# Kernel tuning notes

Hardware: AMD Instinct MI355X
Metric: run time of the kernel (lower is better)

Reference implementation:

```python
import jax, jax.numpy as jnp
import numpy as np

# SSD prior config (small VGGLite-style)
FEATURE_MAPS = [10, 5, 3, 1]
BOXES_PER_LOC = [4, 4, 4, 4]
IMG = 128      # ssd_config.DATA.SHAPE[0] -> WhereTransformer image_size
OBJ = 64
ZWHAT = 64
HID = 512
B = 4
N_OBJ = sum(f * f for f in FEATURE_MAPS)                       # 135
N_FEAT = sum(b * f * f for f, b in zip(FEATURE_MAPS, BOXES_PER_LOC))  # 540


def reconstruction_indices():
    # Replicates Decoder.reconstruction_indices: map per-location latents to per-box slots.
    idx = []
    last = 0
    for f, bpl in zip(FEATURE_MAPS, BOXES_PER_LOC):
        for i in range(f * f):
            idx.extend([last + i] * bpl)
        last += f * f
    return np.asarray(idx, dtype=np.int32)


def what_decode(z, W1, b1, W2, b2):
    # WhatDecoder: MLP z_what -> 3xOBJxOBJ object glyph in (0,1)
    h = jax.nn.relu(z @ W1 + b1)
    return jax.nn.sigmoid(h @ W2 + b2).reshape(-1, 3, OBJ, OBJ)


def where_stn(imgs, zw):
    # WhereTransformer: paste each object image into its (cx, cy, w, h) box on an IMGxIMG canvas
    # via inverse-affine bilinear sampling with zero padding (STN / grid_sample semantics).
    cx, cy, w, h = zw[:, 0], zw[:, 1], zw[:, 2], zw[:, 3]
    w = jnp.maximum(w, 1e-2)
    h = jnp.maximum(h, 1e-2)
    lin = jnp.linspace(-1.0, 1.0, IMG)
    gy, gx = jnp.meshgrid(lin, lin, indexing='ij')           # (IMG, IMG)
    u = (gx[None] - (2.0 * cx - 1.0)[:, None, None]) / w[:, None, None]
    v = (gy[None] - (2.0 * cy - 1.0)[:, None, None]) / h[:, None, None]
    px = (u + 1.0) * 0.5 * (OBJ - 1)                          # (N, IMG, IMG)
    py = (v + 1.0) * 0.5 * (OBJ - 1)

    def sample_one(img, py, px):  # img: (3, OBJ, OBJ)
        x0 = jnp.floor(px); y0 = jnp.floor(py)
        wx = px - x0; wy = py - y0
        x0i = x0.astype(jnp.int32); y0i = y0.astype(jnp.int32)

        def tap(yi, xi, wgt):
            valid = (yi >= 0) & (yi < OBJ) & (xi >= 0) & (xi < OBJ)
            yc = jnp.clip(yi, 0, OBJ - 1)
            xc = jnp.clip(xi, 0, OBJ - 1)
            return img[:, yc, xc] * (wgt * valid)[None]

        return (tap(y0i, x0i, (1 - wy) * (1 - wx)) + tap(y0i, x0i + 1, (1 - wy) * wx)
                + tap(y0i + 1, x0i, wy * (1 - wx)) + tap(y0i + 1, x0i + 1, wy * wx))

    return jax.vmap(sample_one)(imgs, py, px)                 # (N, 3, IMG, IMG)


def setup_inputs() -> dict:
    key = jax.random.key(0)
    ks = jax.random.split(key, 8)
    return {
        'z_what': jax.random.normal(ks[0], (B, N_OBJ, ZWHAT), jnp.float32),
        'z_where': jax.random.uniform(ks[1], (B, N_FEAT, 4), jnp.float32),
        'z_depth': jax.random.normal(ks[2], (B, N_OBJ, 1), jnp.float32),
        'W1': jax.random.normal(ks[3], (ZWHAT, HID), jnp.float32) * 0.05,
        'b1': jnp.zeros((HID,), jnp.float32),
        'W2': jax.random.normal(ks[4], (HID, 3 * OBJ * OBJ), jnp.float32) * 0.02,
        'b2': jnp.zeros((3 * OBJ * OBJ,), jnp.float32),
        'z_present': jax.random.randint(ks[5], (B, N_FEAT, 1), 0, 2, jnp.int32),
    }


def reference(z_what, z_where, z_depth, W1, b1, W2, b2, z_present):
    idx = jnp.asarray(reconstruction_indices())
    # index_select: replicate per-location latents across boxes-per-location
    zw_full = z_what[:, idx]                                  # (B, N_FEAT, ZWHAT)
    zd_full = z_depth[:, idx]                                 # (B, N_FEAT, 1)
    # sort descending by depth; gather all latents in that order
    order = jnp.argsort(-zd_full[..., 0], axis=1)             # (B, N_FEAT)
    s_what = jnp.take_along_axis(zw_full, order[..., None], axis=1)
    s_where = jnp.take_along_axis(z_where, order[..., None], axis=1)
    s_pres = jnp.take_along_axis(z_present, order[..., None], axis=1)
    # decode + STN warp all objects; absent objects are zeroed (equivalent to the
    dec = what_decode(s_what.reshape(-1, ZWHAT), W1, b1, W2, b2)
    warped = where_stn(dec, s_where.reshape(-1, 4))
    imgs = warped.reshape(B, N_FEAT, 3, IMG, IMG) * s_pres.astype(warped.dtype)[..., None, None]
    # depth compositing: per channel-pixel, take the first nonzero value in sorted order
    nz = imgs != 0
    first = jnp.argmax(nz, axis=1)                            # (B, 3, IMG, IMG)
    out = jnp.take_along_axis(imgs, first[:, None], axis=1)[:, 0] * nz.any(axis=1)
    return out
```

## Files before the change

kernel.cpp:

```cpp
#include <hip/hip_runtime.h>
#include <hip/hip_bf16.h>
#include <math.h>

#define NBOX  540
#define NOBJ  135
#define ZW    64
#define HIDN  512
#define NOUT  12288
#define OBJS  64
#define BATCH 4

#define ROLE_WIN   256
#define ROLE_G1    540
#define ROLE_CVT   ((NOUT / 64) * (HIDN / 64))
#define PRE_BLOCKS (ROLE_WIN + ROLE_G1 + ROLE_CVT)

#define OFF_NROWS  0u
#define OFF_USED   256u
#define OFF_REMAP  2560u
#define OFF_ROWOBJ 4864u
#define OFF_PXWIN  7680u
#define OFF_HBF    269824u
#define OFF_W2T    925184u
#define OFF_DEC    13508096u

typedef short  bf16x8 __attribute__((ext_vector_type(8)));
typedef float  f32x4  __attribute__((ext_vector_type(4)));

struct F4 { float x, y, z, w; };

#define GLOAD_LDS16(gp, lp)                                                    \
  __builtin_amdgcn_global_load_lds(                                            \
      (const __attribute__((address_space(1))) void*)(gp),                     \
      (__attribute__((address_space(3))) void*)(lp), 16, 0, 0)

__device__ __forceinline__ unsigned short f2bf(float x) {
  __hip_bfloat16 h = __float2bfloat16(x);
  return *(unsigned short*)&h;
}

__global__ __launch_bounds__(256) void k_pre(
    const float* __restrict__ z_depth,
    const float* __restrict__ z_where,
    const int*   __restrict__ z_present,
    const float* __restrict__ Z,
    const float* __restrict__ W1,
    const float* __restrict__ b1,
    const float* __restrict__ W2,
    int* __restrict__ nrowsp,
    int* __restrict__ used,
    int* __restrict__ remap,
    int* __restrict__ rowobj,
    int* __restrict__ pxwin,
    unsigned short* __restrict__ Hbf,
    unsigned short* __restrict__ W2T)
{
  __shared__ union ShMem {
    struct {
      unsigned long long keys[256];
      F4       cf[NBOX];
      unsigned cbb[NBOX];
      int      cbx[NBOX];
    } win;
    unsigned T[64 * 36];
    float    zs[ZW];
  } u;
  __shared__ int wsums[4], woff[4], nPs;

  const int bid = blockIdx.x;
  const int t   = threadIdx.x;

  if (bid < ROLE_WIN) {
#pragma clang fp contract(off)
    const int b    = bid >> 6;
    const int tile = bid & 63;
    const int lane = t & 63, wv = t >> 6;
    const int y = (tile >> 3) * 16 + (t >> 4);
    const int x = (tile & 7) * 16 + (t & 15);

    unsigned long long key = ~0ull;
    if (t < NOBJ) {
      unsigned uu = __float_as_uint(z_depth[b * NOBJ + t]);
      uu = (uu & 0x80000000u) ? ~uu : (uu | 0x80000000u);
      key = ((unsigned long long)(~uu) << 32) | (unsigned)t;
    }
    u.win.keys[t] = key;
    __syncthreads();
    for (int k = 2; k <= 256; k <<= 1) {
      for (int j = k >> 1; j > 0; j >>= 1) {
        int ixj = t ^ j;
        if (ixj > t) {
          unsigned long long a = u.win.keys[t], c = u.win.keys[ixj];
          bool asc = (t & k) == 0;
          if (asc ? (a > c) : (a < c)) { u.win.keys[t] = c; u.win.keys[ixj] = a; }
        }
        __syncthreads();
      }
    }

    int boxq[3], presq[3], cnt = 0;
#pragma unroll
    for (int q = 0; q < 3; q++) {
      int e = 3 * t + q;
      presq[q] = 0; boxq[q] = 0;
      if (e < NBOX) {
        int o  = (int)(u.win.keys[e >> 2] & 0xFFFFFFFFull);
        int bx = o * 4 + (e & 3);
        boxq[q]  = bx;
        presq[q] = (z_present[b * NBOX + bx] != 0) ? 1 : 0;
        cnt += presq[q];
      }
    }
    int incl = cnt;
#pragma unroll
    for (int o = 1; o < 64; o <<= 1) {
      int vprev = __shfl_up(incl, o, 64);
      if (lane >= o) incl += vprev;
    }
    if (lane == 63) wsums[wv] = incl;
    __syncthreads();
    if (t == 0) {
      int a = 0;
#pragma unroll
      for (int i = 0; i < 4; i++) { woff[i] = a; a += wsums[i]; }
      nPs = a;
    }
    __syncthreads();
    int slot = woff[wv] + incl - cnt;
#pragma unroll
    for (int q = 0; q < 3; q++) {
      if (presq[q]) {
        int bx = boxq[q];
        F4 p = *(const F4*)&z_where[((size_t)b * NBOX + bx) * 4];
        double w  = fmax((double)p.z, 0.01);
        double h  = fmax((double)p.w, 0.01);
        double tx = 2.0 * (double)p.x - 1.0;
        double ty = 2.0 * (double)p.y - 1.0;
        const double S = 65.0 / 63.0;
        int xlo = (int)floor((tx - w * S + 1.0) * 63.5) - 1;
        int xhi = (int)floor((tx + w * S + 1.0) * 63.5) + 2;
        int ylo = (int)floor((ty - h * S + 1.0) * 63.5) - 1;
        int yhi = (int)floor((ty + h * S + 1.0) * 63.5) + 2;
        xlo = max(xlo, 0); ylo = max(ylo, 0);
        xhi = min(xhi, 127); yhi = min(yhi, 127);
        unsigned bb = (xhi < xlo || yhi < ylo) ? 0xFFu
                    : ((unsigned)xlo | ((unsigned)xhi << 8) |
                       ((unsigned)ylo << 16) | ((unsigned)yhi << 24));
        F4 f;
        f.x = (float)tx; f.y = (float)ty;
        f.z = (float)(w * S); f.w = (float)(h * S);
        u.win.cf[slot]  = f;
        u.win.cbb[slot] = bb;
        u.win.cbx[slot] = bx;
        slot++;
      }
    }
    __syncthreads();

    const int nP = nPs;
    const double step = 2.0 / 127.0;
    const double gx = (x == 127) ? 1.0 : ((double)x * step + (-1.0));
    const double gy = (y == 127) ? 1.0 : ((double)y * step + (-1.0));
    const float gxf = (float)gx, gyf = (float)gy;
    const int tx0 = (tile & 7) * 16, tx1 = tx0 + 15;
    const int wy0 = (tile >> 3) * 16 + wv * 4, wy1 = wy0 + 3;

    bool done = false;
    int  win  = -1;
    for (int j = 0; j < nP; j++) {
      if (__all((int)done)) break;
      unsigned bb = u.win.cbb[j];
      int bxlo = (int)(bb & 255u),         bxhi = (int)((bb >> 8) & 255u);
      int bylo = (int)((bb >> 16) & 255u), byhi = (int)(bb >> 24);
      if (bxhi < tx0 || bxlo > tx1 || byhi < wy0 || bylo > wy1) continue;
      bool newly = false;
      if (!done) {
        F4 f = u.win.cf[j];
        float dx = fabsf(gxf - f.x), dy = fabsf(gyf - f.y);
        bool in_lo = (dx < f.z * 0.9999f - 2e-6f) & (dy < f.w * 0.9999f - 2e-6f);
        bool in_hi = (dx < f.z * 1.0001f + 2e-6f) & (dy < f.w * 1.0001f + 2e-6f);
        bool cov;
        if (in_lo) {
          cov = true;
        } else if (!in_hi) {
          cov = false;
        } else {
          F4 p = *(const F4*)&z_where[((size_t)b * NBOX + u.win.cbx[j]) * 4];
          double w  = fmax((double)p.z, 0.01);
          double h  = fmax((double)p.w, 0.01);
          double tx = 2.0 * (double)p.x - 1.0;
          double ty = 2.0 * (double)p.y - 1.0;
          double uu = (gx - tx) / w;
          double vv = (gy - ty) / h;
          double px = (uu + 1.0) * 0.5 * 63.0;
          double py = (vv + 1.0) * 0.5 * 63.0;
          cov = (px > -1.0) && (px < 64.0) && (py > -1.0) && (py < 64.0);
        }
        if (cov) { win = u.win.cbx[j]; done = true; newly = true; }
      }
      unsigned long long nm = __ballot((int)newly);
      if (nm != 0ull && lane == (int)__builtin_ctzll(nm)) {
        int oi = b * NOBJ + (win >> 2);
        if (atomicCAS(&used[oi], 0, 1) == 0) {
          int rr = atomicAdd(nrowsp, 1);
          rowobj[rr] = oi;
          remap[oi]  = rr;
        }
      }
    }
    pxwin[b * 16384 + y * 128 + x] = win;
  } else if (bid < ROLE_WIN + ROLE_G1) {
    const int r = bid - ROLE_WIN;
    if (t < ZW) u.zs[t] = Z[(size_t)r * ZW + t];
    __syncthreads();
    float a0 = b1[t], a1 = b1[t + 256];
#pragma unroll 8
    for (int k = 0; k < ZW; k++) {
      float z = u.zs[k];
      a0 += z * W1[(size_t)k * HIDN + t];
      a1 += z * W1[(size_t)k * HIDN + t + 256];
    }
    Hbf[(size_t)r * HIDN + t]       = f2bf(fmaxf(a0, 0.f));
    Hbf[(size_t)r * HIDN + t + 256] = f2bf(fmaxf(a1, 0.f));
  } else {
    const int c  = bid - ROLE_WIN - ROLE_G1;
    const int n0 = (c % (NOUT / 64)) * 64;
    const int k0 = (c / (NOUT / 64)) * 64;
#pragma unroll
    for (int p = 0; p < 2; p++) {
      int kp = p * 16 + (t >> 4);
      int n4 = t & 15;
      int k  = k0 + kp * 2;
      float4 a = *(const float4*)&W2[(size_t)k * NOUT + n0 + n4 * 4];
      float4 b = *(const float4*)&W2[(size_t)(k + 1) * NOUT + n0 + n4 * 4];
      u.T[(n4*4 + 0) * 36 + kp] = (unsigned)f2bf(a.x) | ((unsigned)f2bf(b.x) << 16);
      u.T[(n4*4 + 1) * 36 + kp] = (unsigned)f2bf(a.y) | ((unsigned)f2bf(b.y) << 16);
      u.T[(n4*4 + 2) * 36 + kp] = (unsigned)f2bf(a.z) | ((unsigned)f2bf(b.z) << 16);
      u.T[(n4*4 + 3) * 36 + kp] = (unsigned)f2bf(a.w) | ((unsigned)f2bf(b.w) << 16);
    }
    __syncthreads();
#pragma unroll
    for (int p = 0; p < 2; p++) {
      int cc = p * 256 + t;
      int n = cc >> 3, ch = cc & 7;
      uint4 v = *(const uint4*)&u.T[n * 36 + ch * 4];
      *(uint4*)&W2T[(size_t)(n0 + n) * HIDN + k0 + ch * 8] = v;
    }
  }
}

__global__ __launch_bounds__(256) void k_gemm2_mfma(
    const unsigned short* __restrict__ Hbf,
    const unsigned short* __restrict__ W2T,
    const float* __restrict__ b2,
    const int* __restrict__ nrowsp,
    const int* __restrict__ rowobj,
    float* __restrict__ dec)
{
  __shared__ unsigned short As[2][128 * 32];
  __shared__ unsigned short Bs[2][128 * 32];
  const int nr = *nrowsp;
  int bid = (int)blockIdx.x;
  bid = (bid & 7) * 60 + (bid >> 3);
  const int m0 = (bid / 96) * 128;
  if (m0 >= nr) return;
  const int n0 = (bid % 96) * 128;

  const int t    = threadIdx.x;
  const int lane = t & 63, wv = t >> 6;
  const int wm = (wv & 1) * 64, wn = (wv >> 1) * 64;

  const int r0  = t >> 2;
  const int kc0 = (t & 3) ^ (r0 & 3);
  const int r1  = r0 + 64;
  const int kc1 = (t & 3) ^ (r1 & 3);

  const int ga0 = (m0 + r0 < nr) ? rowobj[m0 + r0] : 0;
  const int ga1 = (m0 + r1 < nr) ? rowobj[m0 + r1] : 0;
  const unsigned short* a0p = Hbf + (size_t)ga0 * HIDN + kc0 * 8;
  const unsigned short* a1p = Hbf + (size_t)ga1 * HIDN + kc1 * 8;
  const unsigned short* b0p = W2T + (size_t)(n0 + r0) * HIDN + kc0 * 8;
  const unsigned short* b1p = W2T + (size_t)(n0 + r1) * HIDN + kc1 * 8;

  const int fr = lane & 15;
  const int fj = lane >> 4;
  f32x4 acc[4][4] = {};

#define STAGE(buf, koff)                                                       \
  do {                                                                         \
    GLOAD_LDS16(a0p + (koff), &As[buf][t * 8]);                                \
    GLOAD_LDS16(a1p + (koff), &As[buf][(t + 256) * 8]);                        \
    GLOAD_LDS16(b0p + (koff), &Bs[buf][t * 8]);                                \
    GLOAD_LDS16(b1p + (koff), &Bs[buf][(t + 256) * 8]);                        \
  } while (0)

  STAGE(0, 0);
  __syncthreads();
  int cur = 0;
  for (int kt = 0; kt < HIDN / 32; ++kt) {
    if (kt < HIDN / 32 - 1) STAGE(cur ^ 1, (kt + 1) * 32);
    bf16x8 av[4], bv[4];
#pragma unroll
    for (int mi = 0; mi < 4; mi++) {
      int row = wm + mi * 16 + fr;
      av[mi] = *(const bf16x8*)&As[cur][(row * 4 + (fj ^ (row & 3))) * 8];
    }
#pragma unroll
    for (int ni = 0; ni < 4; ni++) {
      int row = wn + ni * 16 + fr;
      bv[ni] = *(const bf16x8*)&Bs[cur][(row * 4 + (fj ^ (row & 3))) * 8];
    }
#pragma unroll
    for (int mi = 0; mi < 4; mi++)
#pragma unroll
      for (int ni = 0; ni < 4; ni++)
        acc[mi][ni] = __builtin_amdgcn_mfma_f32_16x16x32_bf16(av[mi], bv[ni], acc[mi][ni], 0, 0, 0);
    __syncthreads();
    cur ^= 1;
  }
#undef STAGE

#pragma unroll
  for (int ni = 0; ni < 4; ni++) {
    int col = n0 + wn + ni * 16 + fr;
    float bb = b2[col];
#pragma unroll
    for (int mi = 0; mi < 4; mi++) {
#pragma unroll
      for (int r = 0; r < 4; r++) {
        int row = m0 + wm + mi * 16 + fj * 4 + r;
        float v = acc[mi][ni][r] + bb;
        dec[(size_t)row * NOUT + col] = 1.0f / (1.0f + __expf(-v));
      }
    }
  }
}

__global__ __launch_bounds__(256) void k_composite(
    const int* __restrict__ pxwin, const int* __restrict__ remap,
    const float* __restrict__ z_where, const float* __restrict__ dec,
    float* __restrict__ out)
{
#pragma clang fp contract(off)
  const int bid  = blockIdx.x;
  const int t    = threadIdx.x;
  const int b    = bid >> 6;
  const int tile = bid & 63;
  const int y = (tile >> 3) * 16 + (t >> 4);
  const int x = (tile & 7) * 16 + (t & 15);

  const int win = pxwin[b * 16384 + y * 128 + x];
  float o0 = 0.f, o1 = 0.f, o2 = 0.f;
  if (win >= 0) {
    const F4 p = *(const F4*)&z_where[((size_t)b * NBOX + win) * 4];
    const double step = 2.0 / 127.0;
    const double gx = (x == 127) ? 1.0 : ((double)x * step + (-1.0));
    const double gy = (y == 127) ? 1.0 : ((double)y * step + (-1.0));
    double w = fmax((double)p.z, 0.01);
    double h = fmax((double)p.w, 0.01);
    double tx = 2.0 * (double)p.x - 1.0;
    double ty = 2.0 * (double)p.y - 1.0;
    double u = (gx - tx) / w;
    double v = (gy - ty) / h;
    double px = (u + 1.0) * 0.5 * 63.0;
    double py = (v + 1.0) * 0.5 * 63.0;
    double fx = floor(px), fy = floor(py);
    double wx = px - fx, wy = py - fy;
    int x0 = (int)fx, y0 = (int)fy;
    int x1 = x0 + 1, y1 = y0 + 1;
    bool vx0 = (x0 >= 0) && (x0 < OBJS);
    bool vx1 = (x1 >= 0) && (x1 < OBJS);
    bool vy0 = (y0 >= 0) && (y0 < OBJS);
    bool vy1 = (y1 >= 0) && (y1 < OBJS);
    double w00 = (1.0 - wy) * (1.0 - wx);
    double w01 = (1.0 - wy) * wx;
    double w10 = wy * (1.0 - wx);
    double w11 = wy * wx;
    bool c00 = vy0 && vx0 && (w00 > 0.0);
    bool c01 = vy0 && vx1 && (w01 > 0.0);
    bool c10 = vy1 && vx0 && (w10 > 0.0);
    bool c11 = vy1 && vx1 && (w11 > 0.0);
    const int row = remap[b * NOBJ + (win >> 2)];
    const float* g = dec + (size_t)row * NOUT;
    double s0 = 0.0, s1 = 0.0, s2 = 0.0;
    if (c00) { int o = y0*64 + x0; s0 += g[o]*w00; s1 += g[4096+o]*w00; s2 += g[8192+o]*w00; }
    if (c01) { int o = y0*64 + x1; s0 += g[o]*w01; s1 += g[4096+o]*w01; s2 += g[8192+o]*w01; }
    if (c10) { int o = y1*64 + x0; s0 += g[o]*w10; s1 += g[4096+o]*w10; s2 += g[8192+o]*w10; }
    if (c11) { int o = y1*64 + x1; s0 += g[o]*w11; s1 += g[4096+o]*w11; s2 += g[8192+o]*w11; }
    o0 = (float)s0; o1 = (float)s1; o2 = (float)s2;
  }
  const int ob = b * 3 * 16384 + y * 128 + x;
  out[ob]         = o0;
  out[ob + 16384] = o1;
  out[ob + 32768] = o2;
}

extern "C" void kernel_launch(void* const* d_in, const int* in_sizes, int n_in,
                              void* d_out, int out_size, void* d_ws, size_t ws_size,
                              hipStream_t stream) {
  (void)in_sizes; (void)n_in; (void)out_size; (void)ws_size;
  const float* z_what    = (const float*)d_in[0];
  const float* z_where   = (const float*)d_in[1];
  const float* z_depth   = (const float*)d_in[2];
  const float* W1        = (const float*)d_in[3];
  const float* b1        = (const float*)d_in[4];
  const float* W2        = (const float*)d_in[5];
  const float* b2        = (const float*)d_in[6];
  const int*   z_present = (const int*)d_in[7];
  float* out = (float*)d_out;
  char* ws = (char*)d_ws;

  int*            nrowsp = (int*)(ws + OFF_NROWS);
  int*            used   = (int*)(ws + OFF_USED);
  int*            remap  = (int*)(ws + OFF_REMAP);
  int*            rowobj = (int*)(ws + OFF_ROWOBJ);
  int*            pxwin  = (int*)(ws + OFF_PXWIN);
  unsigned short* Hbf    = (unsigned short*)(ws + OFF_HBF);
  unsigned short* W2T    = (unsigned short*)(ws + OFF_W2T);
  float*          dec    = (float*)(ws + OFF_DEC);

  hipMemsetAsync(ws + OFF_NROWS, 0, 2560, stream);

  k_pre<<<dim3(PRE_BLOCKS), dim3(256), 0, stream>>>(
      z_depth, z_where, z_present, z_what, W1, b1, W2,
      nrowsp, used, remap, rowobj, pxwin, Hbf, W2T);
  k_gemm2_mfma<<<dim3((NOUT / 128) * 5), dim3(256), 0, stream>>>(
      Hbf, W2T, b2, nrowsp, rowobj, dec);
  k_composite<<<dim3(256), dim3(256), 0, stream>>>(pxwin, remap, z_where, dec, out);
}
```

Measured before the change: 123.4 us.

## Read fp32 W2 directly in GEMM2 and drop the W2 bf16 transpose pass

Removes the W2 fp32-to-bf16 transpose role from the preprocessing kernel. The GEMM now streams fp32 W2 tiles straight into LDS and converts them to bf16 on the fly. The N tile shrinks from 128 to 32 columns, so the grid grows to 1920 blocks and each wave does 4 MFMAs per k-step instead of 16. This saves a full write and re-read of a bf16 W2 copy. In exchange, A tiles are reloaded many more times, per-MFMA arithmetic intensity drops, and each k-step does scalar LDS reads plus conversions for B.

```diff
diff --git a/kernel.cpp b/kernel.cpp
--- a/kernel.cpp
+++ b/kernel.cpp
@@ -12,8 +12,9 @@
 
 #define ROLE_WIN   256
 #define ROLE_G1    540
-#define ROLE_CVT   ((NOUT / 64) * (HIDN / 64))
-#define PRE_BLOCKS (ROLE_WIN + ROLE_G1 + ROLE_CVT)
+#define PRE_BLOCKS (ROLE_WIN + ROLE_G1)
+
+#define G2_BLOCKS  1920
 
 #define OFF_NROWS  0u
 #define OFF_USED   256u
@@ -21,7 +22,6 @@
 #define OFF_ROWOBJ 4864u
 #define OFF_PXWIN  7680u
 #define OFF_HBF    269824u
-#define OFF_W2T    925184u
 #define OFF_DEC    13508096u
 
 typedef short  bf16x8 __attribute__((ext_vector_type(8)));
@@ -46,14 +46,12 @@
     const float* __restrict__ Z,
     const float* __restrict__ W1,
     const float* __restrict__ b1,
-    const float* __restrict__ W2,
     int* __restrict__ nrowsp,
     int* __restrict__ used,
     int* __restrict__ remap,
     int* __restrict__ rowobj,
     int* __restrict__ pxwin,
-    unsigned short* __restrict__ Hbf,
-    unsigned short* __restrict__ W2T)
+    unsigned short* __restrict__ Hbf)
 {
   __shared__ union ShMem {
     struct {
@@ -62,7 +60,6 @@
       unsigned cbb[NBOX];
       int      cbx[NBOX];
     } win;
-    unsigned T[64 * 36];
     float    zs[ZW];
   } u;
   __shared__ int wsums[4], woff[4], nPs;
@@ -209,7 +206,7 @@
       }
     }
     pxwin[b * 16384 + y * 128 + x] = win;
-  } else if (bid < ROLE_WIN + ROLE_G1) {
+  } else {
     const int r = bid - ROLE_WIN;
     if (t < ZW) u.zs[t] = Z[(size_t)r * ZW + t];
     __syncthreads();
@@ -222,53 +219,30 @@
     }
     Hbf[(size_t)r * HIDN + t]       = f2bf(fmaxf(a0, 0.f));
     Hbf[(size_t)r * HIDN + t + 256] = f2bf(fmaxf(a1, 0.f));
-  } else {
-    const int c  = bid - ROLE_WIN - ROLE_G1;
-    const int n0 = (c % (NOUT / 64)) * 64;
-    const int k0 = (c / (NOUT / 64)) * 64;
-#pragma unroll
-    for (int p = 0; p < 2; p++) {
-      int kp = p * 16 + (t >> 4);
-      int n4 = t & 15;
-      int k  = k0 + kp * 2;
-      float4 a = *(const float4*)&W2[(size_t)k * NOUT + n0 + n4 * 4];
-      float4 b = *(const float4*)&W2[(size_t)(k + 1) * NOUT + n0 + n4 * 4];
-      u.T[(n4*4 + 0) * 36 + kp] = (unsigned)f2bf(a.x) | ((unsigned)f2bf(b.x) << 16);
-      u.T[(n4*4 + 1) * 36 + kp] = (unsigned)f2bf(a.y) | ((unsigned)f2bf(b.y) << 16);
-      u.T[(n4*4 + 2) * 36 + kp] = (unsigned)f2bf(a.z) | ((unsigned)f2bf(b.z) << 16);
-      u.T[(n4*4 + 3) * 36 + kp] = (unsigned)f2bf(a.w) | ((unsigned)f2bf(b.w) << 16);
-    }
-    __syncthreads();
-#pragma unroll
-    for (int p = 0; p < 2; p++) {
-      int cc = p * 256 + t;
-      int n = cc >> 3, ch = cc & 7;
-      uint4 v = *(const uint4*)&u.T[n * 36 + ch * 4];
-      *(uint4*)&W2T[(size_t)(n0 + n) * HIDN + k0 + ch * 8] = v;
-    }
   }
 }
 
 __global__ __launch_bounds__(256) void k_gemm2_mfma(
     const unsigned short* __restrict__ Hbf,
-    const unsigned short* __restrict__ W2T,
+    const float* __restrict__ W2,
     const float* __restrict__ b2,
     const int* __restrict__ nrowsp,
     const int* __restrict__ rowobj,
     float* __restrict__ dec)
 {
   __shared__ unsigned short As[2][128 * 32];
-  __shared__ unsigned short Bs[2][128 * 32];
+  __shared__ float          BsF[2][32 * 32];
   const int nr = *nrowsp;
   int bid = (int)blockIdx.x;
-  bid = (bid & 7) * 60 + (bid >> 3);
-  const int m0 = (bid / 96) * 128;
+  bid = (bid & 7) * 240 + (bid >> 3);
+  const int m0 = (bid % 5) * 128;
   if (m0 >= nr) return;
-  const int n0 = (bid % 96) * 128;
+  const int n0 = (bid / 5) * 32;
 
   const int t    = threadIdx.x;
   const int lane = t & 63, wv = t >> 6;
-  const int wm = (wv & 1) * 64, wn = (wv >> 1) * 64;
+  const int wm = (wv & 1) * 64;
+  const int wn = (wv >> 1) * 16;
 
   const int r0  = t >> 2;
   const int kc0 = (t & 3) ^ (r0 & 3);
@@ -279,59 +253,51 @@
   const int ga1 = (m0 + r1 < nr) ? rowobj[m0 + r1] : 0;
   const unsigned short* a0p = Hbf + (size_t)ga0 * HIDN + kc0 * 8;
   const unsigned short* a1p = Hbf + (size_t)ga1 * HIDN + kc1 * 8;
-  const unsigned short* b0p = W2T + (size_t)(n0 + r0) * HIDN + kc0 * 8;
-  const unsigned short* b1p = W2T + (size_t)(n0 + r1) * HIDN + kc1 * 8;
+  const float* bp = W2 + (size_t)(t >> 3) * NOUT + n0 + (t & 7) * 4;
 
   const int fr = lane & 15;
   const int fj = lane >> 4;
-  f32x4 acc[4][4] = {};
-
-#define STAGE(buf, koff)                                                       \
+  f32x4 acc[4] = {};
+
+#define STAGE(buf, kt)                                                         \
   do {                                                                         \
-    GLOAD_LDS16(a0p + (koff), &As[buf][t * 8]);                                \
-    GLOAD_LDS16(a1p + (koff), &As[buf][(t + 256) * 8]);                        \
-    GLOAD_LDS16(b0p + (koff), &Bs[buf][t * 8]);                                \
-    GLOAD_LDS16(b1p + (koff), &Bs[buf][(t + 256) * 8]);                        \
+    GLOAD_LDS16(a0p + (kt) * 32, &As[buf][t * 8]);                             \
+    GLOAD_LDS16(a1p + (kt) * 32, &As[buf][(t + 256) * 8]);                     \
+    GLOAD_LDS16(bp + (size_t)(kt) * 32 * NOUT, &BsF[buf][t * 4]);              \
   } while (0)
 
   STAGE(0, 0);
   __syncthreads();
   int cur = 0;
   for (int kt = 0; kt < HIDN / 32; ++kt) {
-    if (kt < HIDN / 32 - 1) STAGE(cur ^ 1, (kt + 1) * 32);
-    bf16x8 av[4], bv[4];
+    if (kt < HIDN / 32 - 1) STAGE(cur ^ 1, kt + 1);
+    bf16x8 av[4];
 #pragma unroll
     for (int mi = 0; mi < 4; mi++) {
       int row = wm + mi * 16 + fr;
       av[mi] = *(const bf16x8*)&As[cur][(row * 4 + (fj ^ (row & 3))) * 8];
     }
-#pragma unroll
-    for (int ni = 0; ni < 4; ni++) {
-      int row = wn + ni * 16 + fr;
-      bv[ni] = *(const bf16x8*)&Bs[cur][(row * 4 + (fj ^ (row & 3))) * 8];
-    }
+    bf16x8 bv;
+#pragma unroll
+    for (int j = 0; j < 8; j++)
+      bv[j] = (short)f2bf(BsF[cur][(fj * 8 + j) * 32 + wn + fr]);
 #pragma unroll
     for (int mi = 0; mi < 4; mi++)
-#pragma unroll
-      for (int ni = 0; ni < 4; ni++)
-        acc[mi][ni] = __builtin_amdgcn_mfma_f32_16x16x32_bf16(av[mi], bv[ni], acc[mi][ni], 0, 0, 0);
+      acc[mi] = __builtin_amdgcn_mfma_f32_16x16x32_bf16(av[mi], bv, acc[mi], 0, 0, 0);
     __syncthreads();
     cur ^= 1;
   }
 #undef STAGE
 
-#pragma unroll
-  for (int ni = 0; ni < 4; ni++) {
-    int col = n0 + wn + ni * 16 + fr;
-    float bb = b2[col];
-#pragma unroll
-    for (int mi = 0; mi < 4; mi++) {
-#pragma unroll
-      for (int r = 0; r < 4; r++) {
-        int row = m0 + wm + mi * 16 + fj * 4 + r;
-        float v = acc[mi][ni][r] + bb;
-        dec[(size_t)row * NOUT + col] = 1.0f / (1.0f + __expf(-v));
-      }
+  const int col = n0 + wn + fr;
+  const float bb = b2[col];
+#pragma unroll
+  for (int mi = 0; mi < 4; mi++) {
+#pragma unroll
+    for (int r = 0; r < 4; r++) {
+      int row = m0 + wm + mi * 16 + fj * 4 + r;
+      float v = acc[mi][r] + bb;
+      dec[(size_t)row * NOUT + col] = 1.0f / (1.0f + __expf(-v));
     }
   }
 }
@@ -416,15 +382,14 @@
   int*            rowobj = (int*)(ws + OFF_ROWOBJ);
   int*            pxwin  = (int*)(ws + OFF_PXWIN);
   unsigned short* Hbf    = (unsigned short*)(ws + OFF_HBF);
-  unsigned short* W2T    = (unsigned short*)(ws + OFF_W2T);
   float*          dec    = (float*)(ws + OFF_DEC);
 
   hipMemsetAsync(ws + OFF_NROWS, 0, 2560, stream);
 
   k_pre<<<dim3(PRE_BLOCKS), dim3(256), 0, stream>>>(
-      z_depth, z_where, z_present, z_what, W1, b1, W2,
-      nrowsp, used, remap, rowobj, pxwin, Hbf, W2T);
-  k_gemm2_mfma<<<dim3((NOUT / 128) * 5), dim3(256), 0, stream>>>(
-      Hbf, W2T, b2, nrowsp, rowobj, dec);
+      z_depth, z_where, z_present, z_what, W1, b1,
+      nrowsp, used, remap, rowobj, pxwin, Hbf);
+  k_gemm2_mfma<<<dim3(G2_BLOCKS), dim3(256), 0, stream>>>(
+      Hbf, W2, b2, nrowsp, rowobj, dec);
   k_composite<<<dim3(256), dim3(256), 0, stream>>>(pxwin, remap, z_where, dec, out);
 }
```

After: 118.8 us. -3.7%, faster.
